# Optimization experiments

Measured on AMD Instinct MI355X. Metric: run time of the kernel, lower is better.

Reference implementation:

```python
import jax, jax.numpy as jnp
import numpy as np

NUM_HEADS = 16
B, S, D = 2, 2048, 1024


def setup_inputs() -> dict:
    key = jax.random.key(0)
    ks = jax.random.split(key, 6)
    return {
        "q": jax.random.normal(ks[0], (B, S, D), dtype=jnp.float32),
        "k": jax.random.normal(ks[1], (B, S, D), dtype=jnp.float32),
        "v": jax.random.normal(ks[2], (B, S, D), dtype=jnp.float32),
        "wq": jax.random.normal(ks[3], (D, D), dtype=jnp.float32) * (1.0 / np.sqrt(D)),
        "wk": jax.random.normal(ks[4], (D, D), dtype=jnp.float32) * (1.0 / np.sqrt(D)),
        "wv": jax.random.normal(ks[5], (D, D), dtype=jnp.float32) * (1.0 / np.sqrt(D)),
    }


def reference(q, k, v, wq, wk, wv):
    b, s, d = q.shape
    h = NUM_HEADS
    hd = d // h

    def proj(x, w):
        # torch Linear (no bias): x @ w.T ; chunk(dim=2) == reshape to heads
        return (x @ w.T).reshape(b, s, h, hd).transpose(0, 2, 1, 3)  # [b,h,s,hd]

    qh, kh, vh = proj(q, wq), proj(k, wk), proj(v, wv)
    scale = 1.0 / jnp.sqrt(jnp.asarray(hd, q.dtype))
    scores = jnp.einsum("bhqd,bhkd->bhqk", qh, kh) * scale  # [b,h,s,s]
    # faithful to torch: .tril() zeroes (not -inf) the upper triangle pre-softmax
    mask = jnp.tril(jnp.ones((s, s), dtype=bool))
    scores = jnp.where(mask, scores, jnp.asarray(0.0, scores.dtype))
    attn = jax.nn.softmax(scores, axis=-1)
    out = jnp.einsum("bhqk,bhkd->bhqd", attn, vh)  # [b,h,s,hd]
    return out.transpose(0, 2, 1, 3).reshape(b, s, d)
```

## Files before the change

kernel.cpp:

```cpp
#include <hip/hip_runtime.h>
#include <math.h>

#define B_  2
#define S_  2048
#define D_  1024
#define H_  16
#define HD_ 64
#define NT_ (S_/64)
#define C2_ (0.125f * 1.44269504088896f)

typedef __attribute__((ext_vector_type(8))) _Float16 f16x8;
typedef __attribute__((ext_vector_type(2))) __fp16 h16x2;
typedef __attribute__((ext_vector_type(4))) float f32x4;
typedef unsigned short u16;
typedef unsigned int   u32;

__device__ inline u16 f2h(float f) {
    union { _Float16 h; u16 u; } c; c.h = (_Float16)f;
    return c.u;
}
__device__ inline float h2f(u16 h) {
    union { u16 u; _Float16 h; } c; c.u = h;
    return (float)c.h;
}
__device__ inline u32 pkrtz(float a, float b) {
    union { h16x2 h; u32 u; } c;
    c.h = __builtin_amdgcn_cvt_pkrtz(a, b);
    return c.u;
}

__global__ __launch_bounds__(256)
void precast(const float* __restrict__ wq, const float* __restrict__ wk,
             const float* __restrict__ wv, const float* __restrict__ q,
             const float* __restrict__ k,  const float* __restrict__ v,
             u16* __restrict__ Wq, u16* __restrict__ Wk, u16* __restrict__ Wv,
             u16* __restrict__ Xq, u16* __restrict__ Xk, u16* __restrict__ Xv)
{
    const int z = blockIdx.y;
    const size_t n = (z >= 3) ? (size_t)B_ * S_ * D_ : (size_t)D_ * D_;
    const size_t i = ((size_t)blockIdx.x * 256 + threadIdx.x) * 4;
    if (i >= n) return;
    const float* src = (z == 0) ? wq : (z == 1) ? wk : (z == 2) ? wv
                     : (z == 3) ? q  : (z == 4) ? k  : v;
    u16* dst = (z == 0) ? Wq : (z == 1) ? Wk : (z == 2) ? Wv
             : (z == 3) ? Xq : (z == 4) ? Xk : Xv;
    float4 xv = *(const float4*)&src[i];
    *(ushort4*)&dst[i] = make_ushort4(f2h(xv.x), f2h(xv.y), f2h(xv.z), f2h(xv.w));
}

__global__ __launch_bounds__(256)
void proj_all(const u16* __restrict__ Xq, const u16* __restrict__ Xk,
              const u16* __restrict__ Xv, const u16* __restrict__ Wq,
              const u16* __restrict__ Wk, const u16* __restrict__ Wv,
              u16* __restrict__ QP, u16* __restrict__ KP, u16* __restrict__ VT)
{
    const int z = blockIdx.z;
    const u16* X = (z == 0) ? Xq : (z == 1) ? Xk : Xv;
    const u16* W = (z == 0) ? Wq : (z == 1) ? Wk : Wv;

    __shared__ u16 Xs[128][72];
    __shared__ u16 Ws[128][72];

    const int tid  = threadIdx.x;
    const int w    = tid >> 6;
    const int lane = tid & 63;
    const int quad = lane >> 4;
    const int lr   = lane & 15;
    const int rr   = tid >> 1;
    const int kb   = (tid & 1) * 32;
    const int m0   = blockIdx.y * 128;
    const int n0   = blockIdx.x * 128;

    f32x4 acc[2][8];
    #pragma unroll
    for (int i = 0; i < 2; ++i)
        #pragma unroll
        for (int j = 0; j < 8; ++j) acc[i][j] = (f32x4){0.f, 0.f, 0.f, 0.f};

    for (int k0 = 0; k0 < D_; k0 += 64) {
        f16x8 xv[4], wv[4];
        #pragma unroll
        for (int c = 0; c < 4; ++c) {
            xv[c] = *(const f16x8*)&X[(size_t)(m0 + rr) * D_ + k0 + kb + c * 8];
            wv[c] = *(const f16x8*)&W[(size_t)(n0 + rr) * D_ + k0 + kb + c * 8];
        }
        __syncthreads();
        #pragma unroll
        for (int c = 0; c < 4; ++c) {
            *(f16x8*)&Xs[rr][kb + c * 8] = xv[c];
            *(f16x8*)&Ws[rr][kb + c * 8] = wv[c];
        }
        __syncthreads();

        #pragma unroll
        for (int ch = 0; ch < 2; ++ch) {
            f16x8 a[2];
            #pragma unroll
            for (int i = 0; i < 2; ++i)
                a[i] = *(const f16x8*)&Xs[w * 32 + i * 16 + lr][ch * 32 + quad * 8];
            #pragma unroll
            for (int j = 0; j < 8; ++j) {
                f16x8 b = *(const f16x8*)&Ws[j * 16 + lr][ch * 32 + quad * 8];
                #pragma unroll
                for (int i = 0; i < 2; ++i)
                    acc[i][j] = __builtin_amdgcn_mfma_f32_16x16x32_f16(a[i], b, acc[i][j], 0, 0, 0);
            }
        }
    }

    if (z < 2) {
        u16* P = (z == 0) ? QP : KP;
        const float sc = (z == 0) ? C2_ : 1.0f;
        #pragma unroll
        for (int i = 0; i < 2; ++i)
            #pragma unroll
            for (int j = 0; j < 8; ++j) {
                int n = n0 + j * 16 + lr;
                int h = n >> 6, hd = n & 63;
                #pragma unroll
                for (int r = 0; r < 4; ++r) {
                    int m = m0 + w * 32 + i * 16 + quad * 4 + r;
                    int b = m >> 11, s = m & (S_ - 1);
                    P[(((size_t)b * H_ + h) * S_ + s) * HD_ + hd] = f2h(acc[i][j][r] * sc);
                }
            }
    } else {
        #pragma unroll
        for (int i = 0; i < 2; ++i)
            #pragma unroll
            for (int j = 0; j < 8; ++j) {
                int n  = n0 + j * 16 + lr;
                int h  = n >> 6, vd = n & 63;
                int m  = m0 + w * 32 + i * 16 + quad * 4;
                int b  = m >> 11, s = m & (S_ - 1);
                ushort4 pv = make_ushort4(f2h(acc[i][j][0]), f2h(acc[i][j][1]),
                                          f2h(acc[i][j][2]), f2h(acc[i][j][3]));
                *(ushort4*)&VT[(((size_t)b * H_ + h) * HD_ + vd) * S_ + s] = pv;
            }
    }
}

__global__ __launch_bounds__(64)
void vtilesum_kernel(const u16* __restrict__ VT, float* __restrict__ TS)
{
    const int t = blockIdx.x, bh = blockIdx.y, vd = threadIdx.x;
    const size_t base = ((size_t)bh * HD_ + vd) * S_ + t * 64;
    float acc = 0.f;
    #pragma unroll
    for (int j = 0; j < 64; ++j) acc += h2f(VT[base + j]);
    TS[((size_t)bh * NT_ + t) * HD_ + vd] = acc;
}

__global__ __launch_bounds__(64)
void vsuffix_kernel(const float* __restrict__ TS, float* __restrict__ SUF)
{
    const int bh = blockIdx.x, c = threadIdx.x;
    float acc = 0.f;
    SUF[((size_t)bh * (NT_ + 1) + NT_) * HD_ + c] = 0.f;
    for (int t = NT_ - 1; t >= 0; --t) {
        acc += TS[((size_t)bh * NT_ + t) * HD_ + c];
        SUF[((size_t)bh * (NT_ + 1) + t) * HD_ + c] = acc;
    }
}

__global__ __launch_bounds__(256)
void attn_mfma(const u16* __restrict__ QP, const u16* __restrict__ KP,
               const u16* __restrict__ VT, const float* __restrict__ SUF,
               float* __restrict__ OUT)
{
    const int bh = blockIdx.x;
    const int tq = NT_ - 1 - (int)blockIdx.y;
    const int b  = bh >> 4, h = bh & 15;

    __shared__ u16 Ks[64][72];
    __shared__ u16 Vth[64][72];
    __shared__ u16 Phi[4][16][72];

    const int tid  = threadIdx.x;
    const int w    = tid >> 6;
    const int lane = tid & 63;
    const int quad = lane >> 4;
    const int lr   = lane & 15;
    const int r    = tid >> 2;
    const int cb   = (tid & 3) * 16;

    const u16* Qb = QP + (size_t)bh * S_ * HD_;
    const u16* Kb = KP + (size_t)bh * S_ * HD_;
    const u16* Vb = VT + (size_t)bh * HD_ * S_;

    const int q0 = tq * 64;

    f16x8 qf[2];
    #pragma unroll
    for (int ch = 0; ch < 2; ++ch)
        qf[ch] = *(const f16x8*)(Qb + (size_t)(q0 + w * 16 + lr) * HD_ +
                                 ch * 32 + quad * 8);

    f32x4 of[4];
    #pragma unroll
    for (int n = 0; n < 4; ++n) of[n] = (f32x4){0.f, 0.f, 0.f, 0.f};
    float l_i = 0.f;

    f16x8 kpre[2], vpre[2];
    #pragma unroll
    for (int c = 0; c < 2; ++c) {
        kpre[c] = *(const f16x8*)(Kb + (size_t)r * HD_ + cb + c * 8);
        vpre[c] = *(const f16x8*)(Vb + (size_t)r * S_ + cb + c * 8);
    }

    for (int t = 0; t <= tq; ++t) {
        const int k0t = t * 64;
        __syncthreads();
        #pragma unroll
        for (int c = 0; c < 2; ++c) {
            *(f16x8*)&Ks[r][cb + c * 8]  = kpre[c];
            *(f16x8*)&Vth[r][cb + c * 8] = vpre[c];
        }
        __syncthreads();
        if (t < tq) {
            const int kn = k0t + 64;
            #pragma unroll
            for (int c = 0; c < 2; ++c) {
                kpre[c] = *(const f16x8*)(Kb + (size_t)(kn + r) * HD_ + cb + c * 8);
                vpre[c] = *(const f16x8*)(Vb + (size_t)r * S_ + kn + cb + c * 8);
            }
        }

        f32x4 sf[4];
        #pragma unroll
        for (int f = 0; f < 4; ++f) sf[f] = (f32x4){0.f, 0.f, 0.f, 0.f};
        #pragma unroll
        for (int ch = 0; ch < 2; ++ch)
            #pragma unroll
            for (int f = 0; f < 4; ++f) {
                f16x8 ak = *(const f16x8*)&Ks[f * 16 + lr][ch * 32 + quad * 8];
                sf[f] = __builtin_amdgcn_mfma_f32_16x16x32_f16(ak, qf[ch], sf[f], 0, 0, 0);
            }

        if (t == tq) {
            const int ig = q0 + w * 16 + lr;
            #pragma unroll
            for (int f = 0; f < 4; ++f)
                #pragma unroll
                for (int i = 0; i < 4; ++i) {
                    int jg = k0t + f * 16 + quad * 4 + i;
                    sf[f][i] = (jg <= ig) ? sf[f][i] : 0.f;
                }
        }

        float ps = 0.f;
        #pragma unroll
        for (int f = 0; f < 4; ++f)
            #pragma unroll
            for (int i = 0; i < 4; ++i) {
                float p = exp2f(sf[f][i]);
                sf[f][i] = p;
                ps += p;
            }
        ps += __shfl_xor(ps, 16);
        ps += __shfl_xor(ps, 32);
        l_i += ps;

        #pragma unroll
        for (int f = 0; f < 4; ++f) {
            *(u32*)&Phi[w][lr][f * 16 + quad * 4]     = pkrtz(sf[f][0], sf[f][1]);
            *(u32*)&Phi[w][lr][f * 16 + quad * 4 + 2] = pkrtz(sf[f][2], sf[f][3]);
        }

        #pragma unroll
        for (int ch = 0; ch < 2; ++ch) {
            f16x8 pb = *(const f16x8*)&Phi[w][lr][ch * 32 + quad * 8];
            #pragma unroll
            for (int n = 0; n < 4; ++n) {
                f16x8 av = *(const f16x8*)&Vth[n * 16 + lr][ch * 32 + quad * 8];
                of[n] = __builtin_amdgcn_mfma_f32_16x16x32_f16(av, pb, of[n], 0, 0, 0);
            }
        }
    }

    const int cnt = S_ - (q0 + 64);
    const float* suf = SUF + ((size_t)bh * (NT_ + 1) + (tq + 1)) * HD_;
    float inv = 1.0f / (l_i + (float)cnt);
    const int srow = q0 + w * 16 + lr;
    #pragma unroll
    for (int n = 0; n < 4; ++n) {
        float4 sv = *(const float4*)&suf[n * 16 + quad * 4];
        float4 ov;
        ov.x = (of[n][0] + sv.x) * inv;
        ov.y = (of[n][1] + sv.y) * inv;
        ov.z = (of[n][2] + sv.z) * inv;
        ov.w = (of[n][3] + sv.w) * inv;
        *(float4*)&OUT[((size_t)b * S_ + srow) * D_ + h * HD_ + n * 16 + quad * 4] = ov;
    }
}

extern "C" void kernel_launch(void* const* d_in, const int* in_sizes, int n_in,
                              void* d_out, int out_size, void* d_ws, size_t ws_size,
                              hipStream_t stream)
{
    (void)in_sizes; (void)n_in; (void)out_size; (void)ws_size;
    const float* q  = (const float*)d_in[0];
    const float* k  = (const float*)d_in[1];
    const float* v  = (const float*)d_in[2];
    const float* wq = (const float*)d_in[3];
    const float* wk = (const float*)d_in[4];
    const float* wv = (const float*)d_in[5];
    float* out = (float*)d_out;

    const size_t PROJ = (size_t)B_ * H_ * S_ * HD_;
    const size_t WSZ  = (size_t)D_ * D_;
    u16* QP = (u16*)d_ws;
    u16* KP = QP + PROJ;
    u16* VT = KP + PROJ;
    u16* Xq = VT + PROJ;
    u16* Xk = Xq + PROJ;
    u16* Xv = Xk + PROJ;
    u16* Wq = Xv + PROJ;
    u16* Wk = Wq + WSZ;
    u16* Wv = Wk + WSZ;
    float* TS  = (float*)(Wv + WSZ);
    float* SUF = TS + (size_t)B_ * H_ * NT_ * HD_;

    precast<<<dim3(PROJ / 1024, 6), 256, 0, stream>>>(
        wq, wk, wv, q, k, v, Wq, Wk, Wv, Xq, Xk, Xv);
    proj_all<<<dim3(D_ / 128, (B_ * S_) / 128, 3), 256, 0, stream>>>(
        Xq, Xk, Xv, Wq, Wk, Wv, QP, KP, VT);
    vtilesum_kernel<<<dim3(NT_, B_ * H_), 64, 0, stream>>>(VT, TS);
    vsuffix_kernel<<<B_ * H_, 64, 0, stream>>>(TS, SUF);
    attn_mfma<<<dim3(B_ * H_, NT_), 256, 0, stream>>>(QP, KP, VT, SUF, out);
}
```

Measured before the change: 204.0 us.

## Swizzle projection LDS, prefetch GEMM tiles, pair query tiles per attention block

The projection GEMM now stores its LDS tiles with an XOR swizzle and no padding, and prefetches the next K-slice into registers while the current one is computed. The V tile-sum kernel reads 8 halves per vector load. The attention kernel now runs 512 threads that handle two adjacent query tiles and share each K/V tile load between them, halving K/V global traffic and the number of blocks. The cost is one idle wave group on the last diagonal step, and the lower block count may leave some CUs underused.

Result: no change. 203.2 us (-0.4%).

```diff
diff --git a/kernel.cpp b/kernel.cpp
--- a/kernel.cpp
+++ b/kernel.cpp
@@ -58,8 +58,8 @@
     const u16* X = (z == 0) ? Xq : (z == 1) ? Xk : Xv;
     const u16* W = (z == 0) ? Wq : (z == 1) ? Wk : Wv;
 
-    __shared__ u16 Xs[128][72];
-    __shared__ u16 Ws[128][72];
+    __shared__ u16 Xs[128 * 64];
+    __shared__ u16 Ws[128 * 64];
 
     const int tid  = threadIdx.x;
     const int w    = tid >> 6;
@@ -71,36 +71,52 @@
     const int m0   = blockIdx.y * 128;
     const int n0   = blockIdx.x * 128;
 
+    int woff[4];
+    #pragma unroll
+    for (int c = 0; c < 4; ++c)
+        woff[c] = rr * 64 + ((((kb >> 3) + c) ^ (rr & 7)) << 3);
+
     f32x4 acc[2][8];
     #pragma unroll
     for (int i = 0; i < 2; ++i)
         #pragma unroll
         for (int j = 0; j < 8; ++j) acc[i][j] = (f32x4){0.f, 0.f, 0.f, 0.f};
 
+    f16x8 xv[4], wv[4];
+    #pragma unroll
+    for (int c = 0; c < 4; ++c) {
+        xv[c] = *(const f16x8*)&X[(size_t)(m0 + rr) * D_ + kb + c * 8];
+        wv[c] = *(const f16x8*)&W[(size_t)(n0 + rr) * D_ + kb + c * 8];
+    }
+
     for (int k0 = 0; k0 < D_; k0 += 64) {
-        f16x8 xv[4], wv[4];
+        __syncthreads();
         #pragma unroll
         for (int c = 0; c < 4; ++c) {
-            xv[c] = *(const f16x8*)&X[(size_t)(m0 + rr) * D_ + k0 + kb + c * 8];
-            wv[c] = *(const f16x8*)&W[(size_t)(n0 + rr) * D_ + k0 + kb + c * 8];
+            *(f16x8*)&Xs[woff[c]] = xv[c];
+            *(f16x8*)&Ws[woff[c]] = wv[c];
         }
         __syncthreads();
-        #pragma unroll
-        for (int c = 0; c < 4; ++c) {
-            *(f16x8*)&Xs[rr][kb + c * 8] = xv[c];
-            *(f16x8*)&Ws[rr][kb + c * 8] = wv[c];
-        }
-        __syncthreads();
+
+        if (k0 + 64 < D_) {
+            const int kn = k0 + 64 + kb;
+            #pragma unroll
+            for (int c = 0; c < 4; ++c) {
+                xv[c] = *(const f16x8*)&X[(size_t)(m0 + rr) * D_ + kn + c * 8];
+                wv[c] = *(const f16x8*)&W[(size_t)(n0 + rr) * D_ + kn + c * 8];
+            }
+        }
 
         #pragma unroll
         for (int ch = 0; ch < 2; ++ch) {
+            const int sl = ((ch * 4 + quad) ^ (lr & 7)) * 8;
             f16x8 a[2];
             #pragma unroll
             for (int i = 0; i < 2; ++i)
-                a[i] = *(const f16x8*)&Xs[w * 32 + i * 16 + lr][ch * 32 + quad * 8];
+                a[i] = *(const f16x8*)&Xs[(w * 32 + i * 16 + lr) * 64 + sl];
             #pragma unroll
             for (int j = 0; j < 8; ++j) {
-                f16x8 b = *(const f16x8*)&Ws[j * 16 + lr][ch * 32 + quad * 8];
+                f16x8 b = *(const f16x8*)&Ws[(j * 16 + lr) * 64 + sl];
                 #pragma unroll
                 for (int i = 0; i < 2; ++i)
                     acc[i][j] = __builtin_amdgcn_mfma_f32_16x16x32_f16(a[i], b, acc[i][j], 0, 0, 0);
@@ -144,10 +160,14 @@
 void vtilesum_kernel(const u16* __restrict__ VT, float* __restrict__ TS)
 {
     const int t = blockIdx.x, bh = blockIdx.y, vd = threadIdx.x;
-    const size_t base = ((size_t)bh * HD_ + vd) * S_ + t * 64;
+    const u16* p = VT + ((size_t)bh * HD_ + vd) * S_ + t * 64;
     float acc = 0.f;
     #pragma unroll
-    for (int j = 0; j < 64; ++j) acc += h2f(VT[base + j]);
+    for (int c = 0; c < 8; ++c) {
+        f16x8 vv = *(const f16x8*)&p[c * 8];
+        #pragma unroll
+        for (int j = 0; j < 8; ++j) acc += (float)vv[j];
+    }
     TS[((size_t)bh * NT_ + t) * HD_ + vd] = acc;
 }
 
@@ -163,37 +183,41 @@
     }
 }
 
-__global__ __launch_bounds__(256)
+__global__ __launch_bounds__(512)
 void attn_mfma(const u16* __restrict__ QP, const u16* __restrict__ KP,
                const u16* __restrict__ VT, const float* __restrict__ SUF,
                float* __restrict__ OUT)
 {
-    const int bh = blockIdx.x;
-    const int tq = NT_ - 1 - (int)blockIdx.y;
+    const int bh    = blockIdx.x;
+    const int tq_lo = NT_ - 2 - 2 * (int)blockIdx.y;
+    const int tq_hi = tq_lo + 1;
     const int b  = bh >> 4, h = bh & 15;
 
     __shared__ u16 Ks[64][72];
     __shared__ u16 Vth[64][72];
-    __shared__ u16 Phi[4][16][72];
+    __shared__ u16 Phi[8][16][72];
 
     const int tid  = threadIdx.x;
     const int w    = tid >> 6;
+    const int g    = w >> 2;
+    const int ww   = w & 3;
     const int lane = tid & 63;
     const int quad = lane >> 4;
     const int lr   = lane & 15;
-    const int r    = tid >> 2;
-    const int cb   = (tid & 3) * 16;
+    const int r    = tid >> 3;
+    const int cb   = (tid & 7) * 8;
 
     const u16* Qb = QP + (size_t)bh * S_ * HD_;
     const u16* Kb = KP + (size_t)bh * S_ * HD_;
     const u16* Vb = VT + (size_t)bh * HD_ * S_;
 
+    const int tq = tq_lo + g;
     const int q0 = tq * 64;
 
     f16x8 qf[2];
     #pragma unroll
     for (int ch = 0; ch < 2; ++ch)
-        qf[ch] = *(const f16x8*)(Qb + (size_t)(q0 + w * 16 + lr) * HD_ +
+        qf[ch] = *(const f16x8*)(Qb + (size_t)(q0 + ww * 16 + lr) * HD_ +
                                  ch * 32 + quad * 8);
 
     f32x4 of[4];
@@ -201,79 +225,72 @@
     for (int n = 0; n < 4; ++n) of[n] = (f32x4){0.f, 0.f, 0.f, 0.f};
     float l_i = 0.f;
 
-    f16x8 kpre[2], vpre[2];
-    #pragma unroll
-    for (int c = 0; c < 2; ++c) {
-        kpre[c] = *(const f16x8*)(Kb + (size_t)r * HD_ + cb + c * 8);
-        vpre[c] = *(const f16x8*)(Vb + (size_t)r * S_ + cb + c * 8);
-    }
-
-    for (int t = 0; t <= tq; ++t) {
+    f16x8 kpre, vpre;
+    kpre = *(const f16x8*)(Kb + (size_t)r * HD_ + cb);
+    vpre = *(const f16x8*)(Vb + (size_t)r * S_ + cb);
+
+    for (int t = 0; t <= tq_hi; ++t) {
         const int k0t = t * 64;
         __syncthreads();
-        #pragma unroll
-        for (int c = 0; c < 2; ++c) {
-            *(f16x8*)&Ks[r][cb + c * 8]  = kpre[c];
-            *(f16x8*)&Vth[r][cb + c * 8] = vpre[c];
-        }
+        *(f16x8*)&Ks[r][cb]  = kpre;
+        *(f16x8*)&Vth[r][cb] = vpre;
         __syncthreads();
-        if (t < tq) {
+        if (t < tq_hi) {
             const int kn = k0t + 64;
-            #pragma unroll
-            for (int c = 0; c < 2; ++c) {
-                kpre[c] = *(const f16x8*)(Kb + (size_t)(kn + r) * HD_ + cb + c * 8);
-                vpre[c] = *(const f16x8*)(Vb + (size_t)r * S_ + kn + cb + c * 8);
-            }
-        }
-
-        f32x4 sf[4];
-        #pragma unroll
-        for (int f = 0; f < 4; ++f) sf[f] = (f32x4){0.f, 0.f, 0.f, 0.f};
-        #pragma unroll
-        for (int ch = 0; ch < 2; ++ch)
+            kpre = *(const f16x8*)(Kb + (size_t)(kn + r) * HD_ + cb);
+            vpre = *(const f16x8*)(Vb + (size_t)r * S_ + kn + cb);
+        }
+
+        if (t <= tq) {
+            f32x4 sf[4];
+            #pragma unroll
+            for (int f = 0; f < 4; ++f) sf[f] = (f32x4){0.f, 0.f, 0.f, 0.f};
+            #pragma unroll
+            for (int ch = 0; ch < 2; ++ch)
+                #pragma unroll
+                for (int f = 0; f < 4; ++f) {
+                    f16x8 ak = *(const f16x8*)&Ks[f * 16 + lr][ch * 32 + quad * 8];
+                    sf[f] = __builtin_amdgcn_mfma_f32_16x16x32_f16(ak, qf[ch], sf[f], 0, 0, 0);
+                }
+
+            if (t == tq) {
+                const int ig = q0 + ww * 16 + lr;
+                #pragma unroll
+                for (int f = 0; f < 4; ++f)
+                    #pragma unroll
+                    for (int i = 0; i < 4; ++i) {
+                        int jg = k0t + f * 16 + quad * 4 + i;
+                        sf[f][i] = (jg <= ig) ? sf[f][i] : 0.f;
+                    }
+            }
+
+            float ps = 0.f;
+            #pragma unroll
+            for (int f = 0; f < 4; ++f)
+                #pragma unroll
+                for (int i = 0; i < 4; ++i) {
+                    float p = exp2f(sf[f][i]);
+                    sf[f][i] = p;
+                    ps += p;
+                }
+            ps += __shfl_xor(ps, 16);
+            ps += __shfl_xor(ps, 32);
+            l_i += ps;
+
             #pragma unroll
             for (int f = 0; f < 4; ++f) {
-                f16x8 ak = *(const f16x8*)&Ks[f * 16 + lr][ch * 32 + quad * 8];
-                sf[f] = __builtin_amdgcn_mfma_f32_16x16x32_f16(ak, qf[ch], sf[f], 0, 0, 0);
-            }
-
-        if (t == tq) {
-            const int ig = q0 + w * 16 + lr;
-            #pragma unroll
-            for (int f = 0; f < 4; ++f)
-                #pragma unroll
-                for (int i = 0; i < 4; ++i) {
-                    int jg = k0t + f * 16 + quad * 4 + i;
-                    sf[f][i] = (jg <= ig) ? sf[f][i] : 0.f;
+                *(u32*)&Phi[w][lr][f * 16 + quad * 4]     = pkrtz(sf[f][0], sf[f][1]);
+                *(u32*)&Phi[w][lr][f * 16 + quad * 4 + 2] = pkrtz(sf[f][2], sf[f][3]);
+            }
+
+            #pragma unroll
+            for (int ch = 0; ch < 2; ++ch) {
+                f16x8 pb = *(const f16x8*)&Phi[w][lr][ch * 32 + quad * 8];
+                #pragma unroll
+                for (int n = 0; n < 4; ++n) {
+                    f16x8 av = *(const f16x8*)&Vth[n * 16 + lr][ch * 32 + quad * 8];
+                    of[n] = __builtin_amdgcn_mfma_f32_16x16x32_f16(av, pb, of[n], 0, 0, 0);
                 }
-        }
-
-        float ps = 0.f;
-        #pragma unroll
-        for (int f = 0; f < 4; ++f)
-            #pragma unroll
-            for (int i = 0; i < 4; ++i) {
-                float p = exp2f(sf[f][i]);
-                sf[f][i] = p;
-                ps += p;
-            }
-        ps += __shfl_xor(ps, 16);
-        ps += __shfl_xor(ps, 32);
-        l_i += ps;
-
-        #pragma unroll
-        for (int f = 0; f < 4; ++f) {
-            *(u32*)&Phi[w][lr][f * 16 + quad * 4]     = pkrtz(sf[f][0], sf[f][1]);
-            *(u32*)&Phi[w][lr][f * 16 + quad * 4 + 2] = pkrtz(sf[f][2], sf[f][3]);
-        }
-
-        #pragma unroll
-        for (int ch = 0; ch < 2; ++ch) {
-            f16x8 pb = *(const f16x8*)&Phi[w][lr][ch * 32 + quad * 8];
-            #pragma unroll
-            for (int n = 0; n < 4; ++n) {
-                f16x8 av = *(const f16x8*)&Vth[n * 16 + lr][ch * 32 + quad * 8];
-                of[n] = __builtin_amdgcn_mfma_f32_16x16x32_f16(av, pb, of[n], 0, 0, 0);
             }
         }
     }
@@ -281,7 +298,7 @@
     const int cnt = S_ - (q0 + 64);
     const float* suf = SUF + ((size_t)bh * (NT_ + 1) + (tq + 1)) * HD_;
     float inv = 1.0f / (l_i + (float)cnt);
-    const int srow = q0 + w * 16 + lr;
+    const int srow = q0 + ww * 16 + lr;
     #pragma unroll
     for (int n = 0; n < 4; ++n) {
         float4 sv = *(const float4*)&suf[n * 16 + quad * 4];
@@ -327,5 +344,5 @@
         Xq, Xk, Xv, Wq, Wk, Wv, QP, KP, VT);
     vtilesum_kernel<<<dim3(NT_, B_ * H_), 64, 0, stream>>>(VT, TS);
     vsuffix_kernel<<<B_ * H_, 64, 0, stream>>>(TS, SUF);
-    attn_mfma<<<dim3(B_ * H_, NT_), 256, 0, stream>>>(QP, KP, VT, SUF, out);
-}
+    attn_mfma<<<dim3(B_ * H_, NT_ / 2), 512, 0, stream>>>(QP, KP, VT, SUF, out);
+}
```
